# Kernel optimization log

Measured on AMD Instinct MI355X. Metric: run time of the kernel, lower is better.

Reference implementation:

```python
import jax, jax.numpy as jnp
import numpy as np

B, M, N, D, H = 4, 8, 128, 32, 64
SMALL_V = 1e-8


def setup_inputs() -> dict:
    key = jax.random.key(0)
    ks = jax.random.split(key, 12)
    s = 0.05
    x = jax.random.normal(ks[0], (B, M, N, D), jnp.float32)
    sizes = jax.random.randint(ks[1], (B,), N // 2, N + 1)
    valid = (jnp.arange(N)[None, :] < sizes[:, None]).astype(jnp.float32)  # [B,N]
    x = x * valid[:, None, :, None]  # zero out padded items
    return {
        "x": x,
        "x_size": sizes.astype(jnp.float32),
        "W1a": jax.random.normal(ks[2], (D, 2 * D), jnp.float32) * s,
        "b1a": jax.random.normal(ks[3], (2 * D,), jnp.float32) * s,
        "W1b": jax.random.normal(ks[4], (2 * D, D), jnp.float32) * s,
        "b1b": jax.random.normal(ks[5], (D,), jnp.float32) * s,
        "W2a": jax.random.normal(ks[6], (D, 2 * D), jnp.float32) * s,
        "b2a": jax.random.normal(ks[7], (2 * D,), jnp.float32) * s,
        "W2b": jax.random.normal(ks[8], (2 * D, H), jnp.float32) * s,
        "b2b": jax.random.normal(ks[9], (H,), jnp.float32) * s,
        "w3": jax.random.normal(ks[10], (H,), jnp.float32) * s,
        "b3": jax.random.normal(ks[11], (1,), jnp.float32) * s,
    }


def _item_mask(x):
    # 1.0 where the item's feature row has any nonzero entry, else 0.0. [...,N,1]
    return jnp.any(x != 0, axis=-1, keepdims=True).astype(x.dtype)


def _set_norm(x, x_size):
    # layer_normalization with is_set_norm=True: normalize over (N*D) per set,
    # dividing by the true valid size x_size*D and masking padded items.
    b, m, n, d = x.shape
    mask = jnp.broadcast_to(_item_mask(x), x.shape).reshape(b, m, n * d)
    xr = x.reshape(b, m, n * d)
    denom = x_size[:, None] * d  # [B,1] -> broadcasts over nSet
    mean = jnp.sum(xr, axis=-1) / denom  # [B,M]
    diff = xr - mean[..., None]
    std = jnp.sqrt(jnp.sum(diff * diff * mask, axis=-1) / denom)  # [B,M]
    out = diff / (std[..., None] + SMALL_V) * mask
    return out.reshape(b, m, n, d)


def reference(x, x_size, W1a, b1a, W1b, b1b, W2a, b2a, W2b, b2b, w3, b3):
    mask = _item_mask(x)  # [B,M,N,1]
    x_orig = x
    xn = _set_norm(x, x_size) * mask  # [B,M,N,D]
    # MLP1 (rank-4 -> masked by its own input's item mask)
    m1 = _item_mask(xn)
    x1 = (jnp.matmul(jax.nn.gelu(jnp.matmul(xn, W1a) + b1a), W1b) + b1b) * m1
    # pairwise differences: x_diff[b,m,i,j,:] = x1[b,m,i,:] - xn[b,m,j,:]
    x_diff = x1[:, :, :, None, :] - xn[:, :, None, :, :]  # [B,M,N,N,D]
    # MLP2 (rank-5 -> no mask, is_SoftMax=0)
    e = jnp.matmul(jax.nn.gelu(jnp.matmul(x_diff, W2a) + b2a), W2b) + b2b  # [B,M,N,N,H]
    # aggregation: out[b,m,j,h,d] = sum_i e[b,m,i,j,h] * x1[b,m,i,d]
    agg = jnp.einsum('bmijh,bmid->bmjhd', e, x1)
    # MLP3_linear: Dense(1) over H, then squeeze
    out = jnp.einsum('bmjhd,h->bmjd', agg, w3) + b3[0]
    out = (out + x_orig) * mask
    return out
```

## Files before the change

kernel.cpp:

```cpp
#include <hip/hip_runtime.h>

#define BMC 32
#define NNC 128
#define DDC 32
#define KKC 64
constexpr int ND = NNC * DDC;
constexpr int NK = NNC * KKC;
#define SMALLV 1e-8f

__device__ __forceinline__ float gelu_f(float v) {
    float v2 = v * v;
    float p  = fmaf(0.1029432f, v2, 2.3022082f);
    float e  = __builtin_amdgcn_exp2f(v * p);
    float r  = __builtin_amdgcn_rcpf(e + 1.0f);
    return fmaf(-v, r, v);
}

__global__ __launch_bounds__(256) void mlp_kernel(
    const float* __restrict__ x, const float* __restrict__ x_size,
    const float* __restrict__ W1a, const float* __restrict__ b1a,
    const float* __restrict__ W1b, const float* __restrict__ b1b,
    const float* __restrict__ W2a, const float* __restrict__ b2a,
    const float* __restrict__ W2b, const float* __restrict__ b2b,
    const float* __restrict__ w3,
    float* __restrict__ x1g, float* __restrict__ A1g, float* __restrict__ A2t,
    float* __restrict__ v2g, float* __restrict__ c3g)
{
    __shared__ float sW1a[DDC * KKC];
    __shared__ float sW1b[KKC * DDC];
    __shared__ float sW2a[DDC * KKC];
    __shared__ float sXn[8 * DDC];
    __shared__ float sH[8 * KKC];
    __shared__ float sX1[8 * DDC];
    __shared__ float sB1a[KKC], sB2a[KKC], sB1b[DDC];
    __shared__ float sAny[NNC];
    __shared__ float sRed[4];

    const int t  = threadIdx.x;
    const int bm = blockIdx.x >> 4;
    const int nt = blockIdx.x & 15;
    const int n0 = nt * 8;
    const int w  = t >> 6;

    {
        const float4* a4 = (const float4*)W1a;
        const float4* b4 = (const float4*)W1b;
        const float4* c4 = (const float4*)W2a;
        float4* sa = (float4*)sW1a; float4* sb = (float4*)sW1b; float4* sc = (float4*)sW2a;
        sa[t] = a4[t]; sa[t + 256] = a4[t + 256];
        sb[t] = b4[t]; sb[t + 256] = b4[t + 256];
        sc[t] = c4[t]; sc[t + 256] = c4[t + 256];
    }
    if (t < KKC) { sB1a[t] = b1a[t]; sB2a[t] = b2a[t]; }
    if (t < DDC) { sB1b[t] = b1b[t]; }
    if (t < NNC) sAny[t] = 0.f;
    __syncthreads();

    const float4* xs4 = (const float4*)(x + (size_t)bm * ND);
    float4 v4[4];
    float lsum = 0.f;
    #pragma unroll
    for (int s = 0; s < 4; ++s) {
        int f = t + s * 256;
        float4 q = xs4[f];
        v4[s] = q;
        lsum += q.x + q.y + q.z + q.w;
        if (q.x != 0.f || q.y != 0.f || q.z != 0.f || q.w != 0.f) sAny[f >> 3] = 1.f;
    }
    #pragma unroll
    for (int off = 32; off; off >>= 1) lsum += __shfl_xor(lsum, off);
    if ((t & 63) == 0) sRed[w] = lsum;
    __syncthreads();
    const float denom = x_size[bm >> 3] * (float)DDC;
    const float mean  = (sRed[0] + sRed[1] + sRed[2] + sRed[3]) / denom;

    float lsq = 0.f;
    #pragma unroll
    for (int s = 0; s < 4; ++s) {
        int f = t + s * 256;
        float mk = sAny[f >> 3];
        float dx = v4[s].x - mean, dy = v4[s].y - mean;
        float dz = v4[s].z - mean, dw = v4[s].w - mean;
        lsq += mk * (dx * dx + dy * dy + dz * dz + dw * dw);
    }
    #pragma unroll
    for (int off = 32; off; off >>= 1) lsq += __shfl_xor(lsq, off);
    __syncthreads();
    if ((t & 63) == 0) sRed[w] = lsq;
    __syncthreads();
    const float sq  = sRed[0] + sRed[1] + sRed[2] + sRed[3];
    const float inv = 1.f / (sqrtf(sq / denom) + SMALLV);

    {
        float xv = x[(size_t)bm * ND + n0 * DDC + t];
        sXn[t] = (xv - mean) * inv * sAny[n0 + (t >> 5)];
    }
    __syncthreads();

    const int k    = t & 63;
    const int slot = w;

    #pragma unroll
    for (int r = 0; r < 2; ++r) {
        int n = slot + r * 4;
        const float* xr = &sXn[n * DDC];
        float acc = sB1a[k];
        #pragma unroll
        for (int d = 0; d < DDC; ++d) acc = fmaf(xr[d], sW1a[d * KKC + k], acc);
        sH[n * KKC + k] = gelu_f(acc);
    }
    __syncthreads();

    {
        const int d2 = t & 31;
        const int n  = t >> 5;
        const float* hr = &sH[n * KKC];
        float acc = sB1b[d2];
        #pragma unroll
        for (int q = 0; q < KKC; ++q) acc = fmaf(hr[q], sW1b[q * DDC + d2], acc);
        float val = acc * sAny[n0 + n];
        sX1[n * DDC + d2] = val;
        x1g[(size_t)bm * ND + (n0 + n) * DDC + d2] = val;
    }
    __syncthreads();

    #pragma unroll
    for (int r = 0; r < 2; ++r) {
        int n = slot + r * 4;
        const float* x1r = &sX1[n * DDC];
        const float* xnr = &sXn[n * DDC];
        float a1 = sB2a[k], a2 = 0.f;
        #pragma unroll
        for (int d = 0; d < DDC; ++d) {
            a1 = fmaf(x1r[d], sW2a[d * KKC + k], a1);
            a2 = fmaf(xnr[d], sW2a[d * KKC + k], a2);
        }
        A1g[(size_t)bm * NK + (n0 + n) * KKC + k] = a1;
        A2t[(size_t)bm * NK + k * NNC + (n0 + n)] = a2;
    }

    if (blockIdx.x == 0) {
        if (t < KKC) {
            float acc = 0.f;
            for (int h = 0; h < KKC; ++h) acc += W2b[t * KKC + h] * w3[h];
            v2g[t] = acc;
        }
        if (t == 0) {
            float acc = 0.f;
            for (int h = 0; h < KKC; ++h) acc += b2b[h] * w3[h];
            c3g[0] = acc;
        }
    }
}

__global__ __launch_bounds__(256) void pair_kernel(
    const float* __restrict__ A1g, const float* __restrict__ A2t,
    const float* __restrict__ x1g, const float* __restrict__ v2g,
    const float* __restrict__ c3g, float* __restrict__ partial)
{
    __shared__ float sS[8 * NNC];
    __shared__ float sX1[8 * DDC];
    const int t    = threadIdx.x;
    const int bm   = blockIdx.x >> 4;
    const int ig   = blockIdx.x & 15;
    const int w    = __builtin_amdgcn_readfirstlane(t >> 6);
    const int lane = t & 63;
    const int jg   = w & 1;
    const int ih   = w >> 1;
    const int ib   = ig * 8 + ih * 4;

    sX1[t] = x1g[(size_t)bm * ND + ig * 8 * DDC + t];

    const float* A2p = A2t + (size_t)bm * NK + jg * 64 + lane;
    float a2r[KKC];
    #pragma unroll
    for (int q = 0; q < KKC; ++q) a2r[q] = A2p[q * NNC];

    const float* a1p0 = A1g + (size_t)bm * NK + (ib + 0) * KKC;
    const float* a1p1 = A1g + (size_t)bm * NK + (ib + 1) * KKC;
    const float* a1p2 = A1g + (size_t)bm * NK + (ib + 2) * KKC;
    const float* a1p3 = A1g + (size_t)bm * NK + (ib + 3) * KKC;
    const float c3 = c3g[0];

    float S0 = c3, S1 = c3, S2 = c3, S3 = c3;
    #pragma unroll
    for (int kk = 0; kk < KKC; ++kk) {
        const float vk = v2g[kk];
        S0 = fmaf(gelu_f(a1p0[kk] - a2r[kk]), vk, S0);
        S1 = fmaf(gelu_f(a1p1[kk] - a2r[kk]), vk, S1);
        S2 = fmaf(gelu_f(a1p2[kk] - a2r[kk]), vk, S2);
        S3 = fmaf(gelu_f(a1p3[kk] - a2r[kk]), vk, S3);
    }
    const int jcol = jg * 64 + lane;
    sS[(ih * 4 + 0) * NNC + jcol] = S0;
    sS[(ih * 4 + 1) * NNC + jcol] = S1;
    sS[(ih * 4 + 2) * NNC + jcol] = S2;
    sS[(ih * 4 + 3) * NNC + jcol] = S3;
    __syncthreads();

    const int j  = t >> 1;
    const int dh = t & 1;
    float acc[16];
    #pragma unroll
    for (int d = 0; d < 16; ++d) acc[d] = 0.f;
    #pragma unroll
    for (int i = 0; i < 8; ++i) {
        float S = sS[i * NNC + j];
        const float4* xf = (const float4*)&sX1[i * DDC + dh * 16];
        #pragma unroll
        for (int q = 0; q < 4; ++q) {
            float4 xv = xf[q];
            acc[q * 4 + 0] = fmaf(S, xv.x, acc[q * 4 + 0]);
            acc[q * 4 + 1] = fmaf(S, xv.y, acc[q * 4 + 1]);
            acc[q * 4 + 2] = fmaf(S, xv.z, acc[q * 4 + 2]);
            acc[q * 4 + 3] = fmaf(S, xv.w, acc[q * 4 + 3]);
        }
    }
    float4* pout = (float4*)(partial + ((size_t)(bm * 16 + ig) * NNC) * DDC + (size_t)t * 16);
    #pragma unroll
    for (int q = 0; q < 4; ++q)
        pout[q] = make_float4(acc[q * 4 + 0], acc[q * 4 + 1], acc[q * 4 + 2], acc[q * 4 + 3]);
}

__global__ __launch_bounds__(256) void final_kernel(
    const float* __restrict__ x, const float* __restrict__ b3,
    const float* __restrict__ partial, float* __restrict__ out)
{
    const int gid = blockIdx.x * 256 + threadIdx.x;
    const int bm  = gid >> 12;
    const int rem = gid & 4095;
    const size_t pb = (size_t)bm * 16 * 4096 + rem;
    float sum = 0.f;
    #pragma unroll
    for (int ig = 0; ig < 16; ++ig) sum += partial[pb + (size_t)ig * 4096];
    float xv = x[gid];
    unsigned long long bal = __ballot(xv != 0.f);
    int lane = threadIdx.x & 63;
    unsigned long long half = (lane < 32) ? (bal & 0xFFFFFFFFull) : (bal >> 32);
    float mk = half ? 1.f : 0.f;
    out[gid] = (sum + b3[0] + xv) * mk;
}

extern "C" void kernel_launch(void* const* d_in, const int* in_sizes, int n_in,
                              void* d_out, int out_size, void* d_ws, size_t ws_size,
                              hipStream_t stream) {
    const float* x      = (const float*)d_in[0];
    const float* x_size = (const float*)d_in[1];
    const float* W1a    = (const float*)d_in[2];
    const float* b1a    = (const float*)d_in[3];
    const float* W1b    = (const float*)d_in[4];
    const float* b1b    = (const float*)d_in[5];
    const float* W2a    = (const float*)d_in[6];
    const float* b2a    = (const float*)d_in[7];
    const float* W2b    = (const float*)d_in[8];
    const float* b2b    = (const float*)d_in[9];
    const float* w3     = (const float*)d_in[10];
    const float* b3     = (const float*)d_in[11];
    float* out = (float*)d_out;

    float* ws      = (float*)d_ws;
    float* x1g     = ws;
    float* A1g     = x1g + (size_t)BMC * ND;
    float* A2t     = A1g + (size_t)BMC * NK;
    float* v2g     = A2t + (size_t)BMC * NK;
    float* c3g     = v2g + KKC;
    float* partial = c3g + 64;

    mlp_kernel<<<BMC * 16, 256, 0, stream>>>(x, x_size,
        W1a, b1a, W1b, b1b, W2a, b2a, W2b, b2b, w3,
        x1g, A1g, A2t, v2g, c3g);
    pair_kernel<<<BMC * 16, 256, 0, stream>>>(A1g, A2t, x1g, v2g, c3g, partial);
    final_kernel<<<512, 256, 0, stream>>>(x, b3, partial, out);
}
```

Baseline: 104.7 us.

## Skip padded pair blocks using set size and stage A1/A2 tiles in LDS

The pair kernel now splits each set into two j-halves per block and returns early for i or j tiles beyond the valid set size taken from x_size. The final kernel sums only the valid i-tile partials and writes zero for masked rows. A2 and A1 tiles are staged in shared memory instead of 64 registers per thread. The v2/c3 precompute is also parallelised across the block. This relies on padded items contributing nothing, which holds because x1 is masked to zero for padded rows. The extra launch grid doubles block count while cutting register pressure.

```diff
diff --git a/kernel.cpp b/kernel.cpp
--- a/kernel.cpp
+++ b/kernel.cpp
@@ -97,12 +97,11 @@
     }
     __syncthreads();
 
-    const int k    = t & 63;
-    const int slot = w;
+    const int k = t & 63;
 
     #pragma unroll
     for (int r = 0; r < 2; ++r) {
-        int n = slot + r * 4;
+        int n = w + r * 4;
         const float* xr = &sXn[n * DDC];
         float acc = sB1a[k];
         #pragma unroll
@@ -126,7 +125,7 @@
 
     #pragma unroll
     for (int r = 0; r < 2; ++r) {
-        int n = slot + r * 4;
+        int n = w + r * 4;
         const float* x1r = &sX1[n * DDC];
         const float* xnr = &sXn[n * DDC];
         float a1 = sB2a[k], a2 = 0.f;
@@ -140,105 +139,130 @@
     }
 
     if (blockIdx.x == 0) {
-        if (t < KKC) {
-            float acc = 0.f;
-            for (int h = 0; h < KKC; ++h) acc += W2b[t * KKC + h] * w3[h];
-            v2g[t] = acc;
-        }
-        if (t == 0) {
-            float acc = 0.f;
-            for (int h = 0; h < KKC; ++h) acc += b2b[h] * w3[h];
-            c3g[0] = acc;
+        int kk = t >> 2, hq = t & 3;
+        float p = 0.f;
+        #pragma unroll
+        for (int h = 0; h < 16; ++h)
+            p = fmaf(W2b[kk * KKC + hq * 16 + h], w3[hq * 16 + h], p);
+        __syncthreads();
+        sH[t] = p;
+        __syncthreads();
+        if (hq == 0) v2g[kk] = sH[t] + sH[t + 1] + sH[t + 2] + sH[t + 3];
+        if (t < 64) {
+            float q = b2b[t] * w3[t];
+            #pragma unroll
+            for (int off = 32; off; off >>= 1) q += __shfl_xor(q, off);
+            if (t == 0) c3g[0] = q;
         }
     }
 }
 
 __global__ __launch_bounds__(256) void pair_kernel(
+    const float* __restrict__ x_size,
     const float* __restrict__ A1g, const float* __restrict__ A2t,
     const float* __restrict__ x1g, const float* __restrict__ v2g,
     const float* __restrict__ c3g, float* __restrict__ partial)
 {
-    __shared__ float sS[8 * NNC];
+    __shared__ float sA2[KKC * 64];
+    __shared__ float sA1[8 * KKC];
     __shared__ float sX1[8 * DDC];
+    __shared__ float sS[8 * 64];
+    __shared__ float sV2[KKC];
+
     const int t    = threadIdx.x;
-    const int bm   = blockIdx.x >> 4;
+    const int bm   = blockIdx.x >> 5;
+    const int jg   = (blockIdx.x >> 4) & 1;
     const int ig   = blockIdx.x & 15;
-    const int w    = __builtin_amdgcn_readfirstlane(t >> 6);
+
+    const int iN = (int)(x_size[bm >> 3] + 0.5f);
+    if (ig * 8 >= iN || jg * 64 >= iN) return;
+
+    const int wv   = t >> 6;
     const int lane = t & 63;
-    const int jg   = w & 1;
-    const int ih   = w >> 1;
-    const int ib   = ig * 8 + ih * 4;
-
-    sX1[t] = x1g[(size_t)bm * ND + ig * 8 * DDC + t];
-
-    const float* A2p = A2t + (size_t)bm * NK + jg * 64 + lane;
-    float a2r[KKC];
-    #pragma unroll
-    for (int q = 0; q < KKC; ++q) a2r[q] = A2p[q * NNC];
-
-    const float* a1p0 = A1g + (size_t)bm * NK + (ib + 0) * KKC;
-    const float* a1p1 = A1g + (size_t)bm * NK + (ib + 1) * KKC;
-    const float* a1p2 = A1g + (size_t)bm * NK + (ib + 2) * KKC;
-    const float* a1p3 = A1g + (size_t)bm * NK + (ib + 3) * KKC;
+
+    {
+        const float* A2b = A2t + (size_t)bm * NK + jg * 64;
+        float4* s4 = (float4*)sA2;
+        #pragma unroll
+        for (int s = 0; s < 4; ++s) {
+            int idx = t + s * 256;
+            int k = idx >> 4, f = idx & 15;
+            s4[idx] = *(const float4*)(A2b + k * NNC + f * 4);
+        }
+    }
+    {
+        const float2* a1s = (const float2*)(A1g + (size_t)bm * NK + ig * 8 * KKC);
+        ((float2*)sA1)[t] = a1s[t];
+        sX1[t] = x1g[(size_t)bm * ND + ig * 8 * DDC + t];
+        if (t < KKC) sV2[t] = v2g[t];
+    }
     const float c3 = c3g[0];
-
-    float S0 = c3, S1 = c3, S2 = c3, S3 = c3;
-    #pragma unroll
-    for (int kk = 0; kk < KKC; ++kk) {
-        const float vk = v2g[kk];
-        S0 = fmaf(gelu_f(a1p0[kk] - a2r[kk]), vk, S0);
-        S1 = fmaf(gelu_f(a1p1[kk] - a2r[kk]), vk, S1);
-        S2 = fmaf(gelu_f(a1p2[kk] - a2r[kk]), vk, S2);
-        S3 = fmaf(gelu_f(a1p3[kk] - a2r[kk]), vk, S3);
-    }
-    const int jcol = jg * 64 + lane;
-    sS[(ih * 4 + 0) * NNC + jcol] = S0;
-    sS[(ih * 4 + 1) * NNC + jcol] = S1;
-    sS[(ih * 4 + 2) * NNC + jcol] = S2;
-    sS[(ih * 4 + 3) * NNC + jcol] = S3;
-    __syncthreads();
-
-    const int j  = t >> 1;
-    const int dh = t & 1;
-    float acc[16];
-    #pragma unroll
-    for (int d = 0; d < 16; ++d) acc[d] = 0.f;
-    #pragma unroll
-    for (int i = 0; i < 8; ++i) {
-        float S = sS[i * NNC + j];
-        const float4* xf = (const float4*)&sX1[i * DDC + dh * 16];
-        #pragma unroll
-        for (int q = 0; q < 4; ++q) {
-            float4 xv = xf[q];
-            acc[q * 4 + 0] = fmaf(S, xv.x, acc[q * 4 + 0]);
-            acc[q * 4 + 1] = fmaf(S, xv.y, acc[q * 4 + 1]);
-            acc[q * 4 + 2] = fmaf(S, xv.z, acc[q * 4 + 2]);
-            acc[q * 4 + 3] = fmaf(S, xv.w, acc[q * 4 + 3]);
-        }
-    }
-    float4* pout = (float4*)(partial + ((size_t)(bm * 16 + ig) * NNC) * DDC + (size_t)t * 16);
-    #pragma unroll
-    for (int q = 0; q < 4; ++q)
-        pout[q] = make_float4(acc[q * 4 + 0], acc[q * 4 + 1], acc[q * 4 + 2], acc[q * 4 + 3]);
+    __syncthreads();
+
+    {
+        const int i0 = wv * 2, i1 = i0 + 1;
+        float S0 = c3, S1 = c3;
+        #pragma unroll 8
+        for (int k = 0; k < KKC; ++k) {
+            float a2v = sA2[k * 64 + lane];
+            float vk  = sV2[k];
+            float a10 = sA1[i0 * KKC + k];
+            float a11 = sA1[i1 * KKC + k];
+            S0 = fmaf(gelu_f(a10 - a2v), vk, S0);
+            S1 = fmaf(gelu_f(a11 - a2v), vk, S1);
+        }
+        sS[i0 * 64 + lane] = S0;
+        sS[i1 * 64 + lane] = S1;
+    }
+    __syncthreads();
+
+    {
+        const int j  = t >> 2;
+        const int dq = t & 3;
+        float acc[8];
+        #pragma unroll
+        for (int d = 0; d < 8; ++d) acc[d] = 0.f;
+        #pragma unroll
+        for (int i = 0; i < 8; ++i) {
+            float Sv = sS[i * 64 + j];
+            const float4* xf = (const float4*)&sX1[i * DDC + dq * 8];
+            float4 xa = xf[0], xb = xf[1];
+            acc[0] = fmaf(Sv, xa.x, acc[0]);
+            acc[1] = fmaf(Sv, xa.y, acc[1]);
+            acc[2] = fmaf(Sv, xa.z, acc[2]);
+            acc[3] = fmaf(Sv, xa.w, acc[3]);
+            acc[4] = fmaf(Sv, xb.x, acc[4]);
+            acc[5] = fmaf(Sv, xb.y, acc[5]);
+            acc[6] = fmaf(Sv, xb.z, acc[6]);
+            acc[7] = fmaf(Sv, xb.w, acc[7]);
+        }
+        float* pb = partial + ((size_t)((bm * 2 + jg) * 16 + ig)) * 2048 + t * 8;
+        ((float4*)pb)[0] = make_float4(acc[0], acc[1], acc[2], acc[3]);
+        ((float4*)pb)[1] = make_float4(acc[4], acc[5], acc[6], acc[7]);
+    }
 }
 
 __global__ __launch_bounds__(256) void final_kernel(
-    const float* __restrict__ x, const float* __restrict__ b3,
+    const float* __restrict__ x, const float* __restrict__ x_size,
+    const float* __restrict__ b3,
     const float* __restrict__ partial, float* __restrict__ out)
 {
     const int gid = blockIdx.x * 256 + threadIdx.x;
     const int bm  = gid >> 12;
     const int rem = gid & 4095;
-    const size_t pb = (size_t)bm * 16 * 4096 + rem;
-    float sum = 0.f;
-    #pragma unroll
-    for (int ig = 0; ig < 16; ++ig) sum += partial[pb + (size_t)ig * 4096];
     float xv = x[gid];
     unsigned long long bal = __ballot(xv != 0.f);
     int lane = threadIdx.x & 63;
     unsigned long long half = (lane < 32) ? (bal & 0xFFFFFFFFull) : (bal >> 32);
-    float mk = half ? 1.f : 0.f;
-    out[gid] = (sum + b3[0] + xv) * mk;
+    if (half == 0ull) { out[gid] = 0.f; return; }
+
+    const int iN  = (int)(x_size[bm >> 3] + 0.5f);
+    const int nig = (iN + 7) >> 3;
+    const int jgp = rem >> 11;
+    const size_t pb = ((size_t)((bm * 2 + jgp) * 16)) * 2048 + (rem & 2047);
+    float sum = 0.f;
+    for (int ig = 0; ig < nig; ++ig) sum += partial[pb + (size_t)ig * 2048];
+    out[gid] = sum + b3[0] + xv;
 }
 
 extern "C" void kernel_launch(void* const* d_in, const int* in_sizes, int n_in,
@@ -269,6 +293,6 @@
     mlp_kernel<<<BMC * 16, 256, 0, stream>>>(x, x_size,
         W1a, b1a, W1b, b1b, W2a, b2a, W2b, b2b, w3,
         x1g, A1g, A2t, v2g, c3g);
-    pair_kernel<<<BMC * 16, 256, 0, stream>>>(A1g, A2t, x1g, v2g, c3g, partial);
-    final_kernel<<<512, 256, 0, stream>>>(x, b3, partial, out);
-}
+    pair_kernel<<<BMC * 32, 256, 0, stream>>>(x_size, A1g, A2t, x1g, v2g, c3g, partial);
+    final_kernel<<<512, 256, 0, stream>>>(x, x_size, b3, partial, out);
+}
```

Result: no change. 104.0 us (-0.6%).
